# Optimization experiments

Hardware: AMD Instinct MI355X
Metric: run time of the kernel (lower is better)

The kernel has to match this reference:

```python
import jax, jax.numpy as jnp
import numpy as np

B, H, SQ, SKV, D = 4, 16, 2048, 2048, 128
SCALE = float(np.sqrt(D))  # scale_factor passed to forward; q_k is divided by it


def setup_inputs() -> dict:
    key = jax.random.key(0)
    kq, kk, kv = jax.random.split(key, 3)
    q = jax.random.normal(kq, (B, H, SQ, D), dtype=jnp.float32)
    k = jax.random.normal(kk, (B, H, SKV, D), dtype=jnp.float32)
    v = jax.random.normal(kv, (B, H, SKV, D), dtype=jnp.float32)
    return {"q": q, "k": k, "v": v}


def reference(q, k, v):
    # q_k = q @ k^T, divided by scale_factor
    scores = jnp.einsum("bhqd,bhkd->bhqk", q, k) / SCALE  # [B,H,Sq,Skv]
    attn = jax.nn.softmax(scores, axis=-1)
    # dropout(p=0.1) is identity in eval/inference mode
    out = jnp.einsum("bhqk,bhkd->bhqd", attn, v)  # [B,H,Sq,D]
    return out
```

## Files before the change

### kernel.cpp

```cpp
#include <hip/hip_runtime.h>
#include <hip/hip_bf16.h>

#define B_ 4
#define H_ 16
#define SQ 2048
#define SKV 2048
#define D_ 128
#define BH (B_*H_)
#define BM 128
#define BN 64
#define NITER (SKV/BN)

typedef __attribute__((ext_vector_type(8))) short bf16x8;
typedef __attribute__((ext_vector_type(4))) float f32x4;
typedef __attribute__((ext_vector_type(16))) float f32x16;

__device__ inline unsigned short f2bf(float f) {
    union { float f; unsigned u; } x{f};
    unsigned r = x.u + 0x7fffu + ((x.u >> 16) & 1u);
    return (unsigned short)(r >> 16);
}

#if defined(__has_builtin) && __has_builtin(__builtin_amdgcn_cvt_pk_bf16_f32)
#define PKBF16(a,b) ({ auto _r = __builtin_amdgcn_cvt_pk_bf16_f32((a),(b)); \
                       unsigned _u; __builtin_memcpy(&_u, &_r, 4); _u; })
#else
#define PKBF16(a,b) ((unsigned)f2bf(a) | ((unsigned)f2bf(b) << 16))
#endif

__device__ inline void gl_lds16(const short* g, short* l) {
    __builtin_amdgcn_global_load_lds((const __attribute__((address_space(1))) unsigned*)g,
                                     (__attribute__((address_space(3))) unsigned*)l,
                                     16, 0, 0);
}

__device__ inline void pl32swap(unsigned &a, unsigned &b) {
#if defined(__has_builtin) && __has_builtin(__builtin_amdgcn_permlane32_swap)
    auto r = __builtin_amdgcn_permlane32_swap((int)a, (int)b, false, false);
    unsigned t[2]; __builtin_memcpy(t, &r, 8);
    a = t[0]; b = t[1];
#else
    int lane = threadIdx.x & 63;
    unsigned ap = __shfl(a, lane ^ 32);
    unsigned bp = __shfl(b, lane ^ 32);
    unsigned X = (lane < 32) ? a : bp;
    unsigned Y = (lane < 32) ? ap : b;
    a = X; b = Y;
#endif
}

__global__ __launch_bounds__(256) void prep(const float* __restrict__ kin,
                                            const float* __restrict__ vin,
                                            short* __restrict__ kbf,
                                            short* __restrict__ vtg) {
    int bx = blockIdx.x, tid = threadIdx.x;
    if (bx < 8192) {
        const float4* s = (const float4*)kin;
        uint2* d = (uint2*)kbf;
        int i = bx * 256 + tid;
        const int HALF = (BH * SKV * D_ / 4) / 2;
#pragma unroll
        for (int h = 0; h < 2; ++h) {
            int j = i + h * HALF;
            float4 a = s[j];
            d[j] = make_uint2(PKBF16(a.x, a.y), PKBF16(a.z, a.w));
        }
    } else {
        int bx2 = bx - 8192;
        int bh = bx2 >> 5;
        int t0 = (bx2 & 31) * 64;
        int cp = tid & 63;
        int g  = tid >> 6;
        const float* src = vin + ((size_t)bh * SKV + t0 + g * 16) * D_ + cp * 2;
        unsigned c0[8], c1[8];
#pragma unroll
        for (int t = 0; t < 8; ++t) {
            float2 a = *(const float2*)(src + (size_t)(2 * t) * D_);
            float2 b = *(const float2*)(src + (size_t)(2 * t + 1) * D_);
            c0[t] = PKBF16(a.x, b.x);
            c1[t] = PKBF16(a.y, b.y);
        }
        short* dst = vtg + ((size_t)bh * D_ + cp * 2) * SKV + t0 + g * 16;
        *(uint4*)(dst)            = *(uint4*)&c0[0];
        *(uint4*)(dst + 8)        = *(uint4*)&c0[4];
        *(uint4*)(dst + SKV)      = *(uint4*)&c1[0];
        *(uint4*)(dst + SKV + 8)  = *(uint4*)&c1[4];
    }
}

__global__ __launch_bounds__(256, 3) void fa_kernel(const float* __restrict__ q,
                                                    const short* __restrict__ kbf,
                                                    const short* __restrict__ vtg,
                                                    float* __restrict__ out) {
    __shared__ short Ksh[64 * 128];
    __shared__ short Vsh[128 * 64];

    const int tid = threadIdx.x;
    const int wave = tid >> 6;
    const int lane = tid & 63;
    const int l32 = lane & 31;
    const int hi  = lane >> 5;

    const int bx = blockIdx.x;
    const int qt = bx & 15;
    const int bh = bx >> 4;
    const int qrow0 = qt * BM + wave * 32;

    const float cscale = 1.4426950408889634f * 0.08838834764831845f;

    bf16x8 qf[8];
    {
        const float* qp = q + ((size_t)bh * SQ + qrow0 + l32) * D_ + hi * 8;
#pragma unroll
        for (int dk = 0; dk < 8; ++dk) {
            float4 a = *(const float4*)(qp + dk * 16);
            float4 b = *(const float4*)(qp + dk * 16 + 4);
            union { unsigned u[4]; bf16x8 v; } f;
            f.u[0] = PKBF16(a.x * cscale, a.y * cscale);
            f.u[1] = PKBF16(a.z * cscale, a.w * cscale);
            f.u[2] = PKBF16(b.x * cscale, b.y * cscale);
            f.u[3] = PKBF16(b.z * cscale, b.w * cscale);
            qf[dk] = f.v;
        }
    }

    f32x16 oacc[4];
#pragma unroll
    for (int dt = 0; dt < 4; ++dt) oacc[dt] = (f32x16)0.f;
    float lsum = 0.f;

    const short* kbase = kbf + (size_t)bh * SKV * D_;
    const short* vbase = vtg + (size_t)bh * D_ * SKV;
    const int krow0 = wave * 4 + (lane >> 4);
    const int kc8 = (lane & 15) ^ krow0;
    const short* kg = kbase + krow0 * 128 + kc8 * 8;
    short* kl = Ksh + wave * 512;
    const int vd0 = wave * 8 + (lane >> 3);
    const int vc = (lane & 7) ^ (lane >> 3);
    const short* vg = vbase + (size_t)vd0 * SKV + vc * 8;
    short* vl = Vsh + wave * 512;

    for (int it = 0; it < NITER; ++it) {
        __syncthreads();
#pragma unroll
        for (int s = 0; s < 4; ++s) {
            gl_lds16(kg + s * 2048, kl + s * 2048);
            gl_lds16(vg + (size_t)s * 32 * SKV, vl + s * 2048);
        }
        kg += BN * D_;
        vg += BN;
        __syncthreads();

#pragma unroll
        for (int kvt = 0; kvt < 2; ++kvt) {
            f32x16 sacc = (f32x16)0.f;
#pragma unroll
            for (int dk = 0; dk < 8; ++dk) {
                bf16x8 kf = *(const bf16x8*)&Ksh[(kvt * 32 + l32) * 128 + (((dk * 2 + hi) ^ (lane & 15)) << 3)];
                sacc = __builtin_amdgcn_mfma_f32_32x32x16_bf16(kf, qf[dk], sacc, 0, 0, 0);
            }

            unsigned u[8];
            float ls = 0.f;
#pragma unroll
            for (int t = 0; t < 8; ++t) {
                float p0 = __builtin_amdgcn_exp2f(sacc[2 * t]);
                float p1 = __builtin_amdgcn_exp2f(sacc[2 * t + 1]);
                ls += p0 + p1;
                u[t] = PKBF16(p0, p1);
            }
            lsum += ls;

            pl32swap(u[0], u[2]);
            pl32swap(u[1], u[3]);
            pl32swap(u[4], u[6]);
            pl32swap(u[5], u[7]);
            union { unsigned w[4]; bf16x8 v; } pf0, pf1;
            pf0.w[0] = u[0]; pf0.w[1] = u[1]; pf0.w[2] = u[2]; pf0.w[3] = u[3];
            pf1.w[0] = u[4]; pf1.w[1] = u[5]; pf1.w[2] = u[6]; pf1.w[3] = u[7];

#pragma unroll
            for (int dt = 0; dt < 4; ++dt) {
                bf16x8 vf0 = *(const bf16x8*)&Vsh[(dt * 32 + l32) * 64 + (((kvt * 4 + hi) ^ (lane & 7)) << 3)];
                oacc[dt] = __builtin_amdgcn_mfma_f32_32x32x16_bf16(vf0, pf0.v, oacc[dt], 0, 0, 0);
                bf16x8 vf1 = *(const bf16x8*)&Vsh[(dt * 32 + l32) * 64 + (((kvt * 4 + 2 + hi) ^ (lane & 7)) << 3)];
                oacc[dt] = __builtin_amdgcn_mfma_f32_32x32x16_bf16(vf1, pf1.v, oacc[dt], 0, 0, 0);
            }
        }
    }

    lsum += __shfl_xor(lsum, 32);
    const float rl = 1.0f / lsum;
    float* op = out + ((size_t)bh * SQ + qrow0 + l32) * D_ + hi * 4;
#pragma unroll
    for (int dt = 0; dt < 4; ++dt)
#pragma unroll
        for (int g = 0; g < 4; ++g) {
            f32x4 v;
            v[0] = oacc[dt][4 * g + 0] * rl;
            v[1] = oacc[dt][4 * g + 1] * rl;
            v[2] = oacc[dt][4 * g + 2] * rl;
            v[3] = oacc[dt][4 * g + 3] * rl;
            *(f32x4*)(op + dt * 32 + g * 8) = v;
        }
}

extern "C" void kernel_launch(void* const* d_in, const int* in_sizes, int n_in,
                              void* d_out, int out_size, void* d_ws, size_t ws_size,
                              hipStream_t stream) {
    const float* q = (const float*)d_in[0];
    const float* k = (const float*)d_in[1];
    const float* v = (const float*)d_in[2];
    float* out = (float*)d_out;

    short* kbf = (short*)d_ws;
    short* vtg = kbf + (size_t)BH * SKV * D_;

    prep<<<8192 + 2048, 256, 0, stream>>>(k, v, kbf, vtg);
    fa_kernel<<<BH * (SQ / BM), 256, 0, stream>>>(q, kbf, vtg, out);
}
```

Baseline: 380.1 us.

## Fuse K/V bf16 conversion and V transpose into attention kernel, drop prep pass

```diff
diff --git a/kernel.cpp b/kernel.cpp
--- a/kernel.cpp
+++ b/kernel.cpp
@@ -28,12 +28,6 @@
 #define PKBF16(a,b) ((unsigned)f2bf(a) | ((unsigned)f2bf(b) << 16))
 #endif
 
-__device__ inline void gl_lds16(const short* g, short* l) {
-    __builtin_amdgcn_global_load_lds((const __attribute__((address_space(1))) unsigned*)g,
-                                     (__attribute__((address_space(3))) unsigned*)l,
-                                     16, 0, 0);
-}
-
 __device__ inline void pl32swap(unsigned &a, unsigned &b) {
 #if defined(__has_builtin) && __has_builtin(__builtin_amdgcn_permlane32_swap)
     auto r = __builtin_amdgcn_permlane32_swap((int)a, (int)b, false, false);
@@ -49,48 +43,9 @@
 #endif
 }
 
-__global__ __launch_bounds__(256) void prep(const float* __restrict__ kin,
-                                            const float* __restrict__ vin,
-                                            short* __restrict__ kbf,
-                                            short* __restrict__ vtg) {
-    int bx = blockIdx.x, tid = threadIdx.x;
-    if (bx < 8192) {
-        const float4* s = (const float4*)kin;
-        uint2* d = (uint2*)kbf;
-        int i = bx * 256 + tid;
-        const int HALF = (BH * SKV * D_ / 4) / 2;
-#pragma unroll
-        for (int h = 0; h < 2; ++h) {
-            int j = i + h * HALF;
-            float4 a = s[j];
-            d[j] = make_uint2(PKBF16(a.x, a.y), PKBF16(a.z, a.w));
-        }
-    } else {
-        int bx2 = bx - 8192;
-        int bh = bx2 >> 5;
-        int t0 = (bx2 & 31) * 64;
-        int cp = tid & 63;
-        int g  = tid >> 6;
-        const float* src = vin + ((size_t)bh * SKV + t0 + g * 16) * D_ + cp * 2;
-        unsigned c0[8], c1[8];
-#pragma unroll
-        for (int t = 0; t < 8; ++t) {
-            float2 a = *(const float2*)(src + (size_t)(2 * t) * D_);
-            float2 b = *(const float2*)(src + (size_t)(2 * t + 1) * D_);
-            c0[t] = PKBF16(a.x, b.x);
-            c1[t] = PKBF16(a.y, b.y);
-        }
-        short* dst = vtg + ((size_t)bh * D_ + cp * 2) * SKV + t0 + g * 16;
-        *(uint4*)(dst)            = *(uint4*)&c0[0];
-        *(uint4*)(dst + 8)        = *(uint4*)&c0[4];
-        *(uint4*)(dst + SKV)      = *(uint4*)&c1[0];
-        *(uint4*)(dst + SKV + 8)  = *(uint4*)&c1[4];
-    }
-}
-
 __global__ __launch_bounds__(256, 3) void fa_kernel(const float* __restrict__ q,
-                                                    const short* __restrict__ kbf,
-                                                    const short* __restrict__ vtg,
+                                                    const float* __restrict__ kin,
+                                                    const float* __restrict__ vin,
                                                     float* __restrict__ out) {
     __shared__ short Ksh[64 * 128];
     __shared__ short Vsh[128 * 64];
@@ -101,7 +56,8 @@
     const int l32 = lane & 31;
     const int hi  = lane >> 5;
 
-    const int bx = blockIdx.x;
+    const int bxo = blockIdx.x;
+    const int bx = ((bxo & 7) << 7) | (bxo >> 3);
     const int qt = bx & 15;
     const int bh = bx >> 4;
     const int qrow0 = qt * BM + wave * 32;
@@ -129,26 +85,48 @@
     for (int dt = 0; dt < 4; ++dt) oacc[dt] = (f32x16)0.f;
     float lsum = 0.f;
 
-    const short* kbase = kbf + (size_t)bh * SKV * D_;
-    const short* vbase = vtg + (size_t)bh * D_ * SKV;
-    const int krow0 = wave * 4 + (lane >> 4);
-    const int kc8 = (lane & 15) ^ krow0;
-    const short* kg = kbase + krow0 * 128 + kc8 * 8;
-    short* kl = Ksh + wave * 512;
-    const int vd0 = wave * 8 + (lane >> 3);
-    const int vc = (lane & 7) ^ (lane >> 3);
-    const short* vg = vbase + (size_t)vd0 * SKV + vc * 8;
-    short* vl = Vsh + wave * 512;
+    const int kr  = wave * 16 + (lane >> 2);
+    const int kd0 = (lane & 3) * 32;
+    const float* kp = kin + ((size_t)bh * SKV + kr) * D_ + kd0;
+    short* const krow = Ksh + kr * 128;
+    const int kr15 = kr & 15;
+    const int vg  = lane >> 3;
+    const int vc0 = wave * 32 + (lane & 7) * 4;
+    const float* vp = vin + ((size_t)bh * SKV + vg * 8) * D_ + vc0;
 
     for (int it = 0; it < NITER; ++it) {
         __syncthreads();
+
+        f32x4 kb[8], vb[8];
 #pragma unroll
-        for (int s = 0; s < 4; ++s) {
-            gl_lds16(kg + s * 2048, kl + s * 2048);
-            gl_lds16(vg + (size_t)s * 32 * SKV, vl + s * 2048);
+        for (int t = 0; t < 8; ++t) kb[t] = *(const f32x4*)(kp + 4 * t);
+#pragma unroll
+        for (int t = 0; t < 8; ++t) vb[t] = *(const f32x4*)(vp + (size_t)t * D_);
+        kp += BN * D_;
+        vp += BN * D_;
+
+#pragma unroll
+        for (int j = 0; j < 4; ++j) {
+            const int cj = (lane & 3) * 4 + j;
+            union { unsigned w[4]; bf16x8 v; } o;
+            o.w[0] = PKBF16(kb[2*j][0], kb[2*j][1]);
+            o.w[1] = PKBF16(kb[2*j][2], kb[2*j][3]);
+            o.w[2] = PKBF16(kb[2*j+1][0], kb[2*j+1][1]);
+            o.w[3] = PKBF16(kb[2*j+1][2], kb[2*j+1][3]);
+            *(bf16x8*)(krow + ((cj ^ kr15) << 3)) = o.v;
         }
-        kg += BN * D_;
-        vg += BN;
+
+#pragma unroll
+        for (int i = 0; i < 4; ++i) {
+            const int d = vc0 + i;
+            union { unsigned w[4]; bf16x8 v; } o;
+            o.w[0] = PKBF16(vb[0][i], vb[1][i]);
+            o.w[1] = PKBF16(vb[2][i], vb[3][i]);
+            o.w[2] = PKBF16(vb[4][i], vb[5][i]);
+            o.w[3] = PKBF16(vb[6][i], vb[7][i]);
+            *(bf16x8*)(Vsh + d * 64 + ((vg ^ (d & 7)) << 3)) = o.v;
+        }
+
         __syncthreads();
 
 #pragma unroll
@@ -213,9 +191,5 @@
     const float* v = (const float*)d_in[2];
     float* out = (float*)d_out;
 
-    short* kbf = (short*)d_ws;
-    short* vtg = kbf + (size_t)BH * SKV * D_;
-
-    prep<<<8192 + 2048, 256, 0, stream>>>(k, v, kbf, vtg);
-    fa_kernel<<<BH * (SQ / BM), 256, 0, stream>>>(q, kbf, vtg, out);
+    fa_kernel<<<BH * (SQ / BM), 256, 0, stream>>>(q, k, v, out);
 }
```

Result: slower. 789.2 us (+107.6%).
